# Kernel optimization log

Measured on AMD Instinct MI355X. Metric: run time of the kernel, lower is better.

## Reference

```python
import jax, jax.numpy as jnp
import numpy as np

H = 16          # num_heads
EPS = 1e-6      # RMSNorm eps


def setup_inputs() -> dict:
    key = jax.random.key(0)
    ks = jax.random.split(key, 5)
    B, N, D = 4, 4096, 1024
    x = jax.random.normal(ks[0], (B, N, D), dtype=jnp.float32)
    q = jax.random.normal(ks[1], (D,), dtype=jnp.float32)
    k = jax.random.normal(ks[2], (D,), dtype=jnp.float32)
    log_decay = jax.random.normal(ks[3], (H,), dtype=jnp.float32)
    norm_weight = jnp.ones((D,), dtype=jnp.float32)
    o_w = jax.random.normal(ks[4], (D, D), dtype=jnp.float32) * 0.02
    return {"x": x, "q": q, "k": k, "log_decay": log_decay,
            "norm_weight": norm_weight, "o_w": o_w}


def reference(x, q, k, log_decay, norm_weight, o_w):
    b, n, dm = x.shape
    dh = dm // H
    qh = q.reshape(H, dh)            # per-head query vector (constant over b, n)
    kh = k.reshape(H, dh)            # per-head key vector
    v = x.reshape(b, n, H, dh)       # values = input tokens
    # exp(logsigmoid(a)) == sigmoid(a): per-head decay in (0, 1)
    lam = jax.nn.sigmoid(log_decay)  # (H,)

    def step(S, v_t):
        # S: (b, H, dh, dh) recurrent state;  v_t: (b, H, dh)
        S = lam[None, :, None, None] * S + kh[None, :, :, None] * v_t[:, :, None, :]
        o_t = jnp.einsum('hd,bhdv->bhv', qh, S)
        return S, o_t

    S0 = jnp.zeros((b, H, dh, dh), dtype=x.dtype)
    _, o = jax.lax.scan(step, S0, jnp.moveaxis(v, 1, 0))  # o: (n, b, H, dh)
    o = jnp.moveaxis(o, 0, 1).reshape(b, n, dm)

    # RMSNorm over the channel dim
    o = o * jax.lax.rsqrt(jnp.mean(o * o, axis=-1, keepdims=True) + EPS) * norm_weight
    # o_proj (no bias)
    return o @ o_w.T
```

## Files before the change

### kernel.cpp

```cpp
#include <hip/hip_runtime.h>
#include <hip/hip_bf16.h>
#include <cstdint>
#include <cstddef>

#define HH   16
#define BB   4
#define NN   4096
#define DD   1024
#define MM   (BB * NN)
#define NC   128
#define LC   32
#define EPSV 1e-6f

typedef short short8 __attribute__((ext_vector_type(8)));
typedef float floatx4 __attribute__((ext_vector_type(4)));

__device__ __forceinline__ void async_copy16(const void* g, void* l) {
    __builtin_amdgcn_global_load_lds(
        (const __attribute__((address_space(1))) void*)g,
        (__attribute__((address_space(3))) void*)l, 16, 0, 0);
}

__device__ __forceinline__ uint2 pack_bf16x4(float a, float b, float c, float d) {
    union { __hip_bfloat16 h[4]; uint2 u; } cv;
    cv.h[0] = __float2bfloat16(a); cv.h[1] = __float2bfloat16(b);
    cv.h[2] = __float2bfloat16(c); cv.h[3] = __float2bfloat16(d);
    return cv.u;
}

__device__ __forceinline__ float sigmoidf(float a) {
    return 1.f / (1.f + expf(-a));
}

__global__ void k_wconv(const float* __restrict__ ow, const float* __restrict__ nw,
                        __hip_bfloat16* __restrict__ wp) {
    size_t i4 = (size_t)blockIdx.x * 256 + threadIdx.x;
    int j = (int)((i4 * 4) & (DD - 1));
    float4 v = ((const float4*)ow)[i4];
    ((uint2*)wp)[i4] = pack_bf16x4(v.x * nw[j], v.y * nw[j + 1],
                                   v.z * nw[j + 2], v.w * nw[j + 3]);
}

__global__ void k_chunk_end(const float* __restrict__ x, const float* __restrict__ ld,
                            float* __restrict__ E) {
    int b = blockIdx.x >> 7, c = blockIdx.x & (NC - 1);
    int j4 = threadIdx.x;
    float lam = sigmoidf(ld[j4 >> 4]);
    const float4* xp = (const float4*)(x + ((size_t)(b * NN + c * LC)) * DD) + j4;
    float4 e = {0.f, 0.f, 0.f, 0.f};
    #pragma unroll
    for (int t = 0; t < LC; ++t) {
        float4 v = xp[(size_t)t * (DD / 4)];
        e.x = fmaf(lam, e.x, v.x); e.y = fmaf(lam, e.y, v.y);
        e.z = fmaf(lam, e.z, v.z); e.w = fmaf(lam, e.w, v.w);
    }
    ((float4*)(E + (size_t)blockIdx.x * DD))[j4] = e;
}

__global__ void k_carry(const float* __restrict__ ld, const float* __restrict__ E,
                        float* __restrict__ P) {
    __shared__ float tile[NC][33];
    int b = blockIdx.x >> 5, jg = blockIdx.x & 31;
    int tid = threadIdx.x;
    int cc = tid >> 5, jj = tid & 31;
    #pragma unroll
    for (int it = 0; it < 16; ++it) {
        int c = it * 8 + cc;
        tile[c][jj] = E[(size_t)(b * NC + c) * DD + jg * 32 + jj];
    }
    __syncthreads();
    if (tid < 32) {
        int j = jg * 32 + tid;
        float lam = sigmoidf(ld[j >> 6]);
        float lamL = lam;
        lamL *= lamL; lamL *= lamL; lamL *= lamL; lamL *= lamL; lamL *= lamL;
        float p = 0.f;
        for (int c = 0; c < NC; ++c) {
            float e = tile[c][tid];
            tile[c][tid] = p;
            p = fmaf(lamL, p, e);
        }
    }
    __syncthreads();
    #pragma unroll
    for (int it = 0; it < 16; ++it) {
        int c = it * 8 + cc;
        P[(size_t)(b * NC + c) * DD + jg * 32 + jj] = tile[c][jj];
    }
}

__global__ void k_scan(const float* __restrict__ x, const float* __restrict__ q,
                       const float* __restrict__ k, const float* __restrict__ ld,
                       const float* __restrict__ P, __hip_bfloat16* __restrict__ obf,
                       float* __restrict__ sumsq) {
    __shared__ float ssq[4][LC];
    int b = blockIdx.x >> 7, c = blockIdx.x & (NC - 1);
    int j4 = threadIdx.x;
    int h = j4 >> 4;
    float lam = sigmoidf(ld[h]);
    float4 q4 = ((const float4*)q)[j4];
    float4 k4 = ((const float4*)k)[j4];
    float ch = q4.x * k4.x + q4.y * k4.y + q4.z * k4.z + q4.w * k4.w;
    #pragma unroll
    for (int off = 1; off < 16; off <<= 1) ch += __shfl_xor(ch, off);
    int row0 = b * NN + c * LC;
    int lane = threadIdx.x & 63, w = threadIdx.x >> 6;
    const float4* xp = (const float4*)(x + (size_t)row0 * DD) + j4;
    float4 y = ((const float4*)(P + (size_t)blockIdx.x * DD))[j4];
    for (int t = 0; t < LC; ++t) {
        float4 v = xp[(size_t)t * (DD / 4)];
        y.x = fmaf(lam, y.x, v.x); y.y = fmaf(lam, y.y, v.y);
        y.z = fmaf(lam, y.z, v.z); y.w = fmaf(lam, y.w, v.w);
        float ox = ch * y.x, oy = ch * y.y, oz = ch * y.z, ow = ch * y.w;
        ((uint2*)(obf + (size_t)(row0 + t) * DD))[j4] = pack_bf16x4(ox, oy, oz, ow);
        float s = ox * ox + oy * oy + oz * oz + ow * ow;
        #pragma unroll
        for (int off = 32; off > 0; off >>= 1) s += __shfl_xor(s, off);
        if (lane == 0) ssq[w][t] = s;
    }
    __syncthreads();
    if (threadIdx.x < LC) {
        int t = threadIdx.x;
        sumsq[row0 + t] = ssq[0][t] + ssq[1][t] + ssq[2][t] + ssq[3][t];
    }
}

#define GEMM_STAGE_A(SLOT, S)                                                  \
  do {                                                                         \
    char* _da = (char*)&lds[SLOT][0][0] + w * 1024;                            \
    _Pragma("unroll") for (int _i = 0; _i < 2; ++_i)                           \
      async_copy16(Ag + (size_t)(m0 + _i * 128 + rr) * 1024 + (S) * 32 + oo * 8, \
                   _da + _i * 8192);                                           \
  } while (0)

#define GEMM_STAGE_B(SLOT, S)                                                  \
  do {                                                                         \
    char* _db = (char*)&lds[SLOT][1][0] + w * 1024;                            \
    _Pragma("unroll") for (int _i = 0; _i < 2; ++_i)                           \
      async_copy16(Wg + (size_t)(n0 + _i * 128 + rr) * 1024 + (S) * 32 + oo * 8, \
                   _db + _i * 8192);                                           \
  } while (0)

#define PHASE_A(SLOT, DO_STAGE, S3)                                            \
  do {                                                                         \
    const short* _a = &lds[SLOT][0][0];                                        \
    const short* _b = &lds[SLOT][1][0];                                        \
    _Pragma("unroll") for (int nt = 0; nt < 4; ++nt)                           \
      bf[nt] = *(const short8*)(_b + (brow_base + nt * 16) * 32 + p_rd * 8);   \
    _Pragma("unroll") for (int mt = 0; mt < 4; ++mt)                           \
      af[mt] = *(const short8*)(_a + (arow_base + mt * 16) * 32 + p_rd * 8);   \
    if (DO_STAGE) GEMM_STAGE_A((S3) & 3, S3);                                  \
    __builtin_amdgcn_s_barrier();                                              \
    asm volatile("s_waitcnt lgkmcnt(0)" ::: "memory");                         \
    __builtin_amdgcn_s_setprio(1);                                             \
    _Pragma("unroll") for (int mt = 0; mt < 4; ++mt) {                         \
      _Pragma("unroll") for (int nt = 0; nt < 4; ++nt)                         \
        acc[mt][nt] = __builtin_amdgcn_mfma_f32_16x16x32_bf16(                 \
            af[mt], bf[nt], acc[mt][nt], 0, 0, 0);                             \
    }                                                                          \
    __builtin_amdgcn_s_setprio(0);                                             \
    __builtin_amdgcn_s_barrier();                                              \
  } while (0)

#define PHASE_B(SLOT, DO_STAGE, S3)                                            \
  do {                                                                         \
    const short* _a = &lds[SLOT][0][0];                                        \
    _Pragma("unroll") for (int mt = 0; mt < 4; ++mt)                           \
      af[mt] = *(const short8*)(_a + (arow_base + 64 + mt * 16) * 32 + p_rd * 8); \
    if (DO_STAGE) GEMM_STAGE_B((S3) & 3, S3);                                  \
    __builtin_amdgcn_s_barrier();                                              \
    asm volatile("s_waitcnt lgkmcnt(0)" ::: "memory");                         \
    __builtin_amdgcn_s_setprio(1);                                             \
    _Pragma("unroll") for (int mt = 0; mt < 4; ++mt) {                         \
      _Pragma("unroll") for (int nt = 0; nt < 4; ++nt)                         \
        acc[4 + mt][nt] = __builtin_amdgcn_mfma_f32_16x16x32_bf16(             \
            af[mt], bf[nt], acc[4 + mt][nt], 0, 0, 0);                         \
    }                                                                          \
    __builtin_amdgcn_s_setprio(0);                                             \
  } while (0)

__launch_bounds__(512, 2)
__global__ void k_gemm(const __hip_bfloat16* __restrict__ A,
                       const __hip_bfloat16* __restrict__ W,
                       const float* __restrict__ sumsq, float* __restrict__ out) {
    __shared__ __attribute__((aligned(16))) short lds[4][2][256 * 32];
    const int tid = threadIdx.x;
    const int lane = tid & 63, w = tid >> 6;
    const int wm = w >> 2, wn = w & 3;
    const int g = blockIdx.x;
    const int xcd = g & 7, idx = g >> 3;
    const int bm = xcd * 8 + (idx >> 2);
    const int bn = idx & 3;
    const int m0 = bm * 256, n0 = bn * 256;
    const short* Ag = (const short*)A;
    const short* Wg = (const short*)W;

    const int rr = tid >> 2;
    const int oo = (tid & 3) ^ ((rr >> 1) & 3);

    const int p_rd = (lane >> 4) ^ (((lane & 15) >> 1) & 3);
    const int arow_base = wm * 128 + (lane & 15);
    const int brow_base = wn * 64 + (lane & 15);

    floatx4 acc[8][4] = {};
    short8 af[4], bf[4];

    GEMM_STAGE_A(0, 0); GEMM_STAGE_B(0, 0);
    GEMM_STAGE_A(1, 1); GEMM_STAGE_B(1, 1);
    GEMM_STAGE_A(2, 2); GEMM_STAGE_B(2, 2);
    asm volatile("s_waitcnt vmcnt(8)" ::: "memory");
    __builtin_amdgcn_s_barrier();

    #pragma unroll 1
    for (int s = 0; s < 29; ++s) {
        PHASE_A(s & 3, 1, s + 3);
        PHASE_B(s & 3, 1, s + 3);
        asm volatile("s_waitcnt vmcnt(8)" ::: "memory");
        __builtin_amdgcn_s_barrier();
    }
    PHASE_A(1, 0, 0); PHASE_B(1, 0, 0);
    asm volatile("s_waitcnt vmcnt(4)" ::: "memory");
    __builtin_amdgcn_s_barrier();
    PHASE_A(2, 0, 0); PHASE_B(2, 0, 0);
    asm volatile("s_waitcnt vmcnt(0)" ::: "memory");
    __builtin_amdgcn_s_barrier();
    PHASE_A(3, 0, 0); PHASE_B(3, 0, 0);

    #pragma unroll
    for (int mt = 0; mt < 8; ++mt) {
        #pragma unroll
        for (int r = 0; r < 4; ++r) {
            int mrow = m0 + wm * 128 + mt * 16 + (lane >> 4) * 4 + r;
            float rs = rsqrtf(sumsq[mrow] * (1.f / 1024.f) + EPSV);
            #pragma unroll
            for (int nt = 0; nt < 4; ++nt) {
                int col = n0 + wn * 64 + nt * 16 + (lane & 15);
                out[(size_t)mrow * 1024 + col] = acc[mt][nt][r] * rs;
            }
        }
    }
}

extern "C" void kernel_launch(void* const* d_in, const int* in_sizes, int n_in,
                              void* d_out, int out_size, void* d_ws, size_t ws_size,
                              hipStream_t stream) {
    const float* x  = (const float*)d_in[0];
    const float* q  = (const float*)d_in[1];
    const float* k  = (const float*)d_in[2];
    const float* ld = (const float*)d_in[3];
    const float* nw = (const float*)d_in[4];
    const float* ow = (const float*)d_in[5];
    float* out = (float*)d_out;

    char* ws = (char*)d_ws;
    float* sumsq = (float*)(ws + 256);
    float* E     = (float*)(ws + 65792);
    float* P     = (float*)(ws + 2162944);
    __hip_bfloat16* Wp  = (__hip_bfloat16*)(ws + 4260096);
    __hip_bfloat16* Obf = (__hip_bfloat16*)(ws + 6357248);

    k_wconv<<<(DD * DD / 4) / 256, 256, 0, stream>>>(ow, nw, Wp);
    k_chunk_end<<<BB * NC, 256, 0, stream>>>(x, ld, E);
    k_carry<<<BB * 32, 256, 0, stream>>>(ld, E, P);
    k_scan<<<BB * NC, 256, 0, stream>>>(x, q, k, ld, P, Obf, sumsq);
    k_gemm<<<(MM / 256) * (DD / 256), 512, 0, stream>>>(Obf, Wp, sumsq, out);
}
```

Baseline: 175.5 us.

## Halve scan chunk length, fuse weight conversion with chunk-end pass, reuse E buffer

Changes the chunked linear-recurrence scan from 128 chunks of 32 to 256 chunks of 16, doubling parallel blocks in the chunk-end and scan kernels and shortening per-block serial loops. The bf16 weight conversion is merged into the chunk-end kernel to save a launch, and carry prefixes are written back into E instead of a separate P buffer. The scan's inner loop is now fully unrolled. The cost is a longer serial carry loop over twice as many chunks and more E traffic.

```diff
diff --git a/kernel.cpp b/kernel.cpp
--- a/kernel.cpp
+++ b/kernel.cpp
@@ -8,8 +8,8 @@
 #define NN   4096
 #define DD   1024
 #define MM   (BB * NN)
-#define NC   128
-#define LC   32
+#define NC   256
+#define LC   16
 #define EPSV 1e-6f
 
 typedef short short8 __attribute__((ext_vector_type(8)));
@@ -32,39 +32,39 @@
     return 1.f / (1.f + expf(-a));
 }
 
-__global__ void k_wconv(const float* __restrict__ ow, const float* __restrict__ nw,
-                        __hip_bfloat16* __restrict__ wp) {
-    size_t i4 = (size_t)blockIdx.x * 256 + threadIdx.x;
-    int j = (int)((i4 * 4) & (DD - 1));
-    float4 v = ((const float4*)ow)[i4];
-    ((uint2*)wp)[i4] = pack_bf16x4(v.x * nw[j], v.y * nw[j + 1],
-                                   v.z * nw[j + 2], v.w * nw[j + 3]);
-}
-
-__global__ void k_chunk_end(const float* __restrict__ x, const float* __restrict__ ld,
-                            float* __restrict__ E) {
-    int b = blockIdx.x >> 7, c = blockIdx.x & (NC - 1);
-    int j4 = threadIdx.x;
-    float lam = sigmoidf(ld[j4 >> 4]);
-    const float4* xp = (const float4*)(x + ((size_t)(b * NN + c * LC)) * DD) + j4;
-    float4 e = {0.f, 0.f, 0.f, 0.f};
-    #pragma unroll
-    for (int t = 0; t < LC; ++t) {
-        float4 v = xp[(size_t)t * (DD / 4)];
-        e.x = fmaf(lam, e.x, v.x); e.y = fmaf(lam, e.y, v.y);
-        e.z = fmaf(lam, e.z, v.z); e.w = fmaf(lam, e.w, v.w);
-    }
-    ((float4*)(E + (size_t)blockIdx.x * DD))[j4] = e;
-}
-
-__global__ void k_carry(const float* __restrict__ ld, const float* __restrict__ E,
-                        float* __restrict__ P) {
+__global__ void k_prep(const float* __restrict__ x, const float* __restrict__ ld,
+                       float* __restrict__ E, const float* __restrict__ ow,
+                       const float* __restrict__ nw, __hip_bfloat16* __restrict__ wp) {
+    int g = blockIdx.x;
+    if (g < BB * NC) {
+        int b = g >> 8, c = g & (NC - 1);
+        int j4 = threadIdx.x;
+        float lam = sigmoidf(ld[j4 >> 4]);
+        const float4* xp = (const float4*)(x + ((size_t)(b * NN + c * LC)) * DD) + j4;
+        float4 e = {0.f, 0.f, 0.f, 0.f};
+        #pragma unroll
+        for (int t = 0; t < LC; ++t) {
+            float4 v = xp[(size_t)t * (DD / 4)];
+            e.x = fmaf(lam, e.x, v.x); e.y = fmaf(lam, e.y, v.y);
+            e.z = fmaf(lam, e.z, v.z); e.w = fmaf(lam, e.w, v.w);
+        }
+        ((float4*)(E + (size_t)g * DD))[j4] = e;
+    } else {
+        size_t i4 = (size_t)(g - BB * NC) * 256 + threadIdx.x;
+        int j = (int)((i4 * 4) & (DD - 1));
+        float4 v = ((const float4*)ow)[i4];
+        ((uint2*)wp)[i4] = pack_bf16x4(v.x * nw[j], v.y * nw[j + 1],
+                                       v.z * nw[j + 2], v.w * nw[j + 3]);
+    }
+}
+
+__global__ void k_carry(const float* __restrict__ ld, float* __restrict__ E) {
     __shared__ float tile[NC][33];
     int b = blockIdx.x >> 5, jg = blockIdx.x & 31;
     int tid = threadIdx.x;
     int cc = tid >> 5, jj = tid & 31;
     #pragma unroll
-    for (int it = 0; it < 16; ++it) {
+    for (int it = 0; it < NC / 8; ++it) {
         int c = it * 8 + cc;
         tile[c][jj] = E[(size_t)(b * NC + c) * DD + jg * 32 + jj];
     }
@@ -73,7 +73,7 @@
         int j = jg * 32 + tid;
         float lam = sigmoidf(ld[j >> 6]);
         float lamL = lam;
-        lamL *= lamL; lamL *= lamL; lamL *= lamL; lamL *= lamL; lamL *= lamL;
+        lamL *= lamL; lamL *= lamL; lamL *= lamL; lamL *= lamL;
         float p = 0.f;
         for (int c = 0; c < NC; ++c) {
             float e = tile[c][tid];
@@ -83,9 +83,9 @@
     }
     __syncthreads();
     #pragma unroll
-    for (int it = 0; it < 16; ++it) {
+    for (int it = 0; it < NC / 8; ++it) {
         int c = it * 8 + cc;
-        P[(size_t)(b * NC + c) * DD + jg * 32 + jj] = tile[c][jj];
+        E[(size_t)(b * NC + c) * DD + jg * 32 + jj] = tile[c][jj];
     }
 }
 
@@ -94,7 +94,7 @@
                        const float* __restrict__ P, __hip_bfloat16* __restrict__ obf,
                        float* __restrict__ sumsq) {
     __shared__ float ssq[4][LC];
-    int b = blockIdx.x >> 7, c = blockIdx.x & (NC - 1);
+    int b = blockIdx.x >> 8, c = blockIdx.x & (NC - 1);
     int j4 = threadIdx.x;
     int h = j4 >> 4;
     float lam = sigmoidf(ld[h]);
@@ -107,6 +107,7 @@
     int lane = threadIdx.x & 63, w = threadIdx.x >> 6;
     const float4* xp = (const float4*)(x + (size_t)row0 * DD) + j4;
     float4 y = ((const float4*)(P + (size_t)blockIdx.x * DD))[j4];
+    #pragma unroll
     for (int t = 0; t < LC; ++t) {
         float4 v = xp[(size_t)t * (DD / 4)];
         y.x = fmaf(lam, y.x, v.x); y.y = fmaf(lam, y.y, v.y);
@@ -255,13 +256,11 @@
     char* ws = (char*)d_ws;
     float* sumsq = (float*)(ws + 256);
     float* E     = (float*)(ws + 65792);
-    float* P     = (float*)(ws + 2162944);
     __hip_bfloat16* Wp  = (__hip_bfloat16*)(ws + 4260096);
     __hip_bfloat16* Obf = (__hip_bfloat16*)(ws + 6357248);
 
-    k_wconv<<<(DD * DD / 4) / 256, 256, 0, stream>>>(ow, nw, Wp);
-    k_chunk_end<<<BB * NC, 256, 0, stream>>>(x, ld, E);
-    k_carry<<<BB * 32, 256, 0, stream>>>(ld, E, P);
-    k_scan<<<BB * NC, 256, 0, stream>>>(x, q, k, ld, P, Obf, sumsq);
+    k_prep<<<BB * NC + (DD * DD / 4) / 256, 256, 0, stream>>>(x, ld, E, ow, nw, Wp);
+    k_carry<<<BB * 32, 256, 0, stream>>>(ld, E);
+    k_scan<<<BB * NC, 256, 0, stream>>>(x, q, k, ld, E, Obf, sumsq);
     k_gemm<<<(MM / 256) * (DD / 256), 512, 0, stream>>>(Obf, Wp, sumsq, out);
 }
```

New measurement: 175.3 us. No clear change (-0.1%).
